# Optimization experiments

Hardware: AMD Instinct MI355X
Metric: run time of the kernel (lower is better)

Reference implementation:

```python
import jax, jax.numpy as jnp
import numpy as np

N = 100000            # number of nodes
E = 1600000           # number of edges (avg degree 16)
D = 32                # embedding dim
MASK_DEPTH = 3        # cfg.mask_depth
PATH_PROB = 0.5       # cfg.path_prob
NUM_MASK_CAND = 1024  # cfg.num_mask_cand
EPS_NORM = 1e-12      # F.normalize eps


def setup_inputs() -> dict:
    key = jax.random.key(0)
    k1, k2 = jax.random.split(key)
    edge_index = jax.random.randint(k1, (2, E), 0, N)  # [2, E] (row, col) COO indices
    adj_values = jnp.ones((E,), dtype=jnp.float32)     # sparse values (binary adjacency)
    embeds = jax.random.normal(k2, (N, D), dtype=jnp.float32)
    return {"edge_index": edge_index, "adj_values": adj_values, "embeds": embeds}


def _spmm(rows, cols, vals, x):
    # out[i] = sum_{e: rows[e]==i} vals[e] * x[cols[e]]  -- irregular gather + scatter-add
    return jax.ops.segment_sum(x[cols] * vals[:, None], rows, num_segments=N)


def _l2_normalize(x):
    n = jnp.sqrt(jnp.sum(x * x, axis=-1, keepdims=True))
    return x / jnp.maximum(n, EPS_NORM)


def reference(edge_index, adj_values, embeds):
    rows, cols = edge_index[0], edge_index[1]
    vals = adj_values

    # order = row-sums of sparse adj, shape [N, 1]
    order = jax.ops.segment_sum(vals, rows, num_segments=N)[:, None]

    fst_emb = _spmm(rows, cols, vals, embeds) - embeds
    fst_num = order
    emb = [fst_emb]
    num = [fst_num]

    drop_key = jax.random.key(42)
    for i in range(MASK_DEPTH):
        # sparse_dropout with keep prob path_prob**(i+1); zeroing values == dropping edges in spmm
        keep_prob = PATH_PROB ** (i + 1)
        u = jax.random.uniform(jax.random.fold_in(drop_key, i), (E,))
        keep = jnp.floor(u + keep_prob)  # 1.0 with prob keep_prob, else 0.0
        vals = vals * keep               # dropout compounds across iterations

        emb.append(_spmm(rows, cols, vals, emb[-1]) - emb[-1] - order * emb[-1])
        num.append(_spmm(rows, cols, vals, num[-1]) - num[-1] - order)
        order = jax.ops.segment_sum(vals, rows, num_segments=N)[:, None]

    subgraph_embeds = sum(emb) / (sum(num) + 1e-8)
    subgraph_embeds = _l2_normalize(subgraph_embeds)
    embeds_n = _l2_normalize(embeds)

    scores = jnp.sum(subgraph_embeds * embeds_n, axis=-1)  # [N]
    # Gumbel noise: -log(-log(U))
    u = jax.random.uniform(jax.random.key(7), (N,))
    scores = scores + (-jnp.log(-jnp.log(u)))

    _, candidates = jax.lax.top_k(scores, NUM_MASK_CAND)
    return scores, candidates
```

## Files before the change

kernel.cpp:

```cpp
#include <hip/hip_runtime.h>
#include <stdint.h>
#include <stddef.h>

#define NN 100000
#define NE 1600000
#define DD 32
#define NCAND 1024
#define HSIZE 65536
#define SORTN 4096
#define NBUK ((NN + 255) / 256)
#define EPB 4096
#define BCAP 5120

#define CAP1 832000
#define CAP2 432000
#define CAP3 240000

__host__ __device__ inline void tf2x32(uint32_t k0, uint32_t k1, uint32_t x0, uint32_t x1,
                                       uint32_t& o0, uint32_t& o1) {
  uint32_t ks2 = k0 ^ k1 ^ 0x1BD11BDAu;
  uint32_t v0 = x0 + k0, v1 = x1 + k1;
#define TFR(r) { v0 += v1; v1 = (v1 << (r)) | (v1 >> (32 - (r))); v1 ^= v0; }
  TFR(13) TFR(15) TFR(26) TFR(6)   v0 += k1;  v1 += ks2 + 1u;
  TFR(17) TFR(29) TFR(16) TFR(24)  v0 += ks2; v1 += k0 + 2u;
  TFR(13) TFR(15) TFR(26) TFR(6)   v0 += k0;  v1 += k1 + 3u;
  TFR(17) TFR(29) TFR(16) TFR(24)  v0 += k1;  v1 += ks2 + 4u;
  TFR(13) TFR(15) TFR(26) TFR(6)   v0 += ks2; v1 += k0 + 5u;
#undef TFR
  o0 = v0; o1 = v1;
}

__device__ __forceinline__ uint32_t jax_bits32(uint32_t k0, uint32_t k1, uint32_t i) {
  uint32_t o0, o1;
  tf2x32(k0, k1, 0u, i, o0, o1);
  return o0 ^ o1;
}

__device__ __forceinline__ float bits_to_uniform(uint32_t b) {
  return __fsub_rn(__uint_as_float((b >> 9) | 0x3f800000u), 1.0f);
}

__device__ __forceinline__ float pairwise32(const float* x) {
  float r[8];
#pragma unroll
  for (int j = 0; j < 8; ++j) r[j] = x[j];
#pragma unroll
  for (int b = 8; b < 32; b += 8)
#pragma unroll
    for (int j = 0; j < 8; ++j) r[j] = __fadd_rn(r[j], x[b + j]);
  float a01 = __fadd_rn(r[0], r[1]), a23 = __fadd_rn(r[2], r[3]);
  float a45 = __fadd_rn(r[4], r[5]), a67 = __fadd_rn(r[6], r[7]);
  return __fadd_rn(__fadd_rn(a01, a23), __fadd_rn(a45, a67));
}


__global__ __launch_bounds__(512) void kA2_bin(
    const int* __restrict__ rows, const int* __restrict__ cols,
    const float* __restrict__ adj,
    uint32_t k00, uint32_t k01, uint32_t k10, uint32_t k11,
    uint32_t k20, uint32_t k21,
    int* __restrict__ bucketCursor, int4* __restrict__ pkBin,
    int* __restrict__ bucketCntS) {
  __shared__ int hist[NBUK];
  __shared__ int base[NBUK];
  __shared__ int h1[NBUK];
  __shared__ int h2[NBUK];
  __shared__ int h3[NBUK];
  __shared__ uint8_t lvs[EPB];
  __shared__ uint16_t rank16[EPB];
  int tid = threadIdx.x;
  for (int i = tid; i < NBUK; i += 512) { hist[i] = 0; h1[i] = 0; h2[i] = 0; h3[i] = 0; }
  __syncthreads();
  int e0 = blockIdx.x * EPB;
  for (int k = 0; k < 8; ++k) {
    int e = e0 + k * 512 + tid;
    int lv = 0;
    if (e < NE) {
      float u0 = bits_to_uniform(jax_bits32(k00, k01, (uint32_t)e));
      float u1 = bits_to_uniform(jax_bits32(k10, k11, (uint32_t)e));
      float u2 = bits_to_uniform(jax_bits32(k20, k21, (uint32_t)e));
      float kp0 = floorf(__fadd_rn(u0, 0.5f));
      float kp1 = floorf(__fadd_rn(u1, 0.25f));
      float kp2 = floorf(__fadd_rn(u2, 0.125f));
      if (kp0 != 0.0f) { lv = 1; if (kp1 != 0.0f) { lv = 2; if (kp2 != 0.0f) lv = 3; } }
      int b = rows[e] >> 8;
      rank16[k * 512 + tid] = (uint16_t)atomicAdd(&hist[b], 1);
      if (lv >= 1) {
        atomicAdd(&h1[b], 1);
        if (lv >= 2) {
          atomicAdd(&h2[b], 1);
          if (lv >= 3) atomicAdd(&h3[b], 1);
        }
      }
    }
    lvs[k * 512 + tid] = (uint8_t)lv;
  }
  __syncthreads();
  for (int i = tid; i < NBUK; i += 512) {
    int h = hist[i];
    base[i] = (h > 0) ? atomicAdd(&bucketCursor[i], h) : 0;
    if (h) atomicAdd(&bucketCntS[i], h);
    if (h1[i]) atomicAdd(&bucketCntS[NBUK + i], h1[i]);
    if (h2[i]) atomicAdd(&bucketCntS[2 * NBUK + i], h2[i]);
    if (h3[i]) atomicAdd(&bucketCntS[3 * NBUK + i], h3[i]);
  }
  __syncthreads();
  for (int k = 0; k < 8; ++k) {
    int e = e0 + k * 512 + tid;
    if (e < NE) {
      int r = rows[e];
      int b = r >> 8;
      int lv = (int)lvs[k * 512 + tid];
      int pos = base[b] + (int)rank16[k * 512 + tid];
      if (pos < BCAP)
        pkBin[(size_t)b * BCAP + pos] =
            make_int4(cols[e], __float_as_int(adj[e]), (e << 2) | lv, r);
    }
  }
}

__global__ __launch_bounds__(512) void k_scanBS(const int* __restrict__ bucketCntS,
                                                int* __restrict__ bucketBaseS) {
  __shared__ int sb[512];
  int a = blockIdx.x;
  const int* c = bucketCntS + (size_t)a * NBUK;
  int* o = bucketBaseS + (size_t)a * (NBUK + 1);
  int tid = threadIdx.x;
  int v = (tid < NBUK) ? c[tid] : 0;
  sb[tid] = v;
  __syncthreads();
  for (int off = 1; off < 512; off <<= 1) {
    int x = (tid >= off) ? sb[tid - off] : 0;
    __syncthreads();
    sb[tid] += x;
    __syncthreads();
  }
  if (tid < NBUK) o[tid] = sb[tid] - v;
  if (tid == NBUK - 1) o[NBUK] = sb[tid];
}

__global__ __launch_bounds__(512) void kB_emit(
    const int* __restrict__ bucketBaseS, const int4* __restrict__ pkBin,
    int* __restrict__ rpAll,
    int2* __restrict__ pk0, int2* __restrict__ pk1,
    int2* __restrict__ pk2, int2* __restrict__ pk3,
    float* __restrict__ order0, float* __restrict__ order1, float* __restrict__ order2) {
  __shared__ unsigned long long cnt64[256];
  __shared__ unsigned long long sb64[256];
  __shared__ unsigned long long ps64[512];
  __shared__ int start0[256];
  __shared__ int cur[256];
  __shared__ uint32_t keyF[BCAP];
  __shared__ int2 payL[BCAP];
  __shared__ uint16_t origG[BCAP];
  int b = blockIdx.x, tid = threadIdx.x;
  int bB0 = bucketBaseS[b];
  int n = bucketBaseS[b + 1] - bB0;
  if (n > BCAP) n = BCAP;
  size_t sRead = (size_t)b * BCAP;
  int r0 = b << 8;
  int nr = NN - r0; if (nr > 256) nr = 256;
  int bB1 = bucketBaseS[(NBUK + 1) + b];
  int bB2 = bucketBaseS[2 * (NBUK + 1) + b];
  int bB3 = bucketBaseS[3 * (NBUK + 1) + b];
  if (tid < 256) { cnt64[tid] = 0ull; cur[tid] = 0; }
  __syncthreads();
  for (int i = tid; i < n; i += 512) {
    int4 p = pkBin[sRead + i];
    int lr = p.w - r0;
    int lv = p.z & 3;
    keyF[i] = ((uint32_t)lr << 23) | (uint32_t)p.z;
    payL[i] = make_int2(p.x, p.y);
    unsigned long long add = 1ull;
    if (lv >= 1) add |= 1ull << 16;
    if (lv >= 2) add |= 1ull << 32;
    if (lv >= 3) add |= 1ull << 48;
    atomicAdd(&cnt64[lr], add);
  }
  __syncthreads();
  unsigned long long own = (tid < 256) ? cnt64[tid] : 0ull;
  if (tid < 256) sb64[tid] = own;
  __syncthreads();
  for (int off = 1; off < 256; off <<= 1) {
    unsigned long long v = (tid < 256 && tid >= off) ? sb64[tid - off] : 0ull;
    __syncthreads();
    if (tid < 256) sb64[tid] += v;
    __syncthreads();
  }
  if (tid < 256) {
    unsigned long long ex = sb64[tid] - own;
    start0[tid] = (int)(ex & 0xFFFFull);
    if (tid < nr) {
      rpAll[r0 + tid] = bB0 + (int)(ex & 0xFFFFull);
      rpAll[(NN + 1) + r0 + tid] = bB1 + (int)((ex >> 16) & 0xFFFFull);
      rpAll[2 * (NN + 1) + r0 + tid] = bB2 + (int)((ex >> 32) & 0xFFFFull);
      rpAll[3 * (NN + 1) + r0 + tid] = bB3 + (int)((ex >> 48) & 0xFFFFull);
    }
  }
  if (b == NBUK - 1 && tid == 0) {
    rpAll[NN] = bucketBaseS[NBUK];
    rpAll[(NN + 1) + NN] = bucketBaseS[(NBUK + 1) + NBUK];
    rpAll[2 * (NN + 1) + NN] = bucketBaseS[2 * (NBUK + 1) + NBUK];
    rpAll[3 * (NN + 1) + NN] = bucketBaseS[3 * (NBUK + 1) + NBUK];
  }
  __syncthreads();
  for (int i = tid; i < n; i += 512) {
    int lr = (int)(keyF[i] >> 23);
    int slot = start0[lr] + atomicAdd(&cur[lr], 1);
    origG[slot] = (uint16_t)i;
  }
  __syncthreads();
  {
    int C2 = (n + 511) >> 9;
    int lo2 = tid * C2, hi2 = lo2 + C2;
    if (lo2 > n) lo2 = n;
    if (hi2 > n) hi2 = n;
    uint16_t vals[10];
    uint16_t pos[10];
    int cntE = 0;
    for (int i = lo2; i < hi2; ++i) {
      uint16_t ov = origG[i];
      uint32_t ki = keyF[ov];
      int lr = (int)(ki >> 23);
      int st = start0[lr];
      int d = (int)(cnt64[lr] & 0xFFFFull);
      int rank = 0;
      for (int j = 0; j < d; ++j) {
        uint32_t kj = keyF[origG[st + j]];
        rank += (kj < ki) ? 1 : 0;
      }
      vals[cntE] = ov;
      pos[cntE] = (uint16_t)(st + rank);
      ++cntE;
    }
    __syncthreads();
    for (int q = 0; q < cntE; ++q) origG[pos[q]] = vals[q];
  }
  __syncthreads();
  if (tid < nr) {
    int d = (int)(cnt64[tid] & 0xFFFFull);
    int st = start0[tid];
    float o0 = 0.0f, o1v = 0.0f, o2v = 0.0f;
    for (int i = 0; i < d; ++i) {
      uint16_t o = origG[st + i];
      int lv = (int)(keyF[o] & 3u);
      float a = __int_as_float(payL[o].y);
      o0 = __fadd_rn(o0, a);
      if (lv >= 1) { o1v = __fadd_rn(o1v, a); if (lv >= 2) o2v = __fadd_rn(o2v, a); }
    }
    order0[r0 + tid] = o0; order1[r0 + tid] = o1v; order2[r0 + tid] = o2v;
  }
  int C = (n + 511) >> 9;
  int lo = tid * C, hi = lo + C;
  if (lo > n) lo = n;
  if (hi > n) hi = n;
  int c1 = 0, c2 = 0, c3 = 0;
  for (int i = lo; i < hi; ++i) {
    int lv = (int)(keyF[origG[i]] & 3u);
    c1 += (lv >= 1); c2 += (lv >= 2); c3 += (lv >= 3);
  }
  unsigned long long mine = (unsigned long long)c1 |
                            ((unsigned long long)c2 << 16) |
                            ((unsigned long long)c3 << 32);
  ps64[tid] = mine;
  __syncthreads();
  for (int off = 1; off < 512; off <<= 1) {
    unsigned long long v = (tid >= off) ? ps64[tid - off] : 0ull;
    __syncthreads();
    ps64[tid] += v;
    __syncthreads();
  }
  unsigned long long ex = ps64[tid] - mine;
  int o1 = bB1 + (int)(ex & 0xFFFFull);
  int o2 = bB2 + (int)((ex >> 16) & 0xFFFFull);
  int o3 = bB3 + (int)((ex >> 32) & 0xFFFFull);
  for (int i = lo; i < hi; ++i) {
    uint16_t o = origG[i];
    int lv = (int)(keyF[o] & 3u);
    int2 pkv = payL[o];
    pk0[bB0 + i] = pkv;
    if (lv >= 1) {
      pk1[o1++] = pkv;
      if (lv >= 2) {
        pk2[o2++] = pkv;
        if (lv >= 3) pk3[o3++] = pkv;
      }
    }
  }
}


__global__ void k_emb0(const int* __restrict__ rp, const int2* __restrict__ pk,
                       const float* __restrict__ embeds, float* __restrict__ e0) {
  int tid = blockIdx.x * blockDim.x + threadIdx.x;
  int r = tid >> 5, d = tid & 31;
  if (r >= NN) return;
  int s = rp[r], t = rp[r + 1];
  float acc = 0.0f;
  for (int base = s; base < t; base += 32) {
    int idx = base + d;
    int2 p = (idx < t) ? pk[idx] : make_int2(0, 0);
    int m = t - base; if (m > 32) m = 32;
    for (int j = 0; j < m; j += 8) {
      int cc[8], aa[8];
      float xx[8];
#pragma unroll
      for (int q = 0; q < 8; ++q) {
        cc[q] = __shfl(p.x, j + q, 32);
        aa[q] = __shfl(p.y, j + q, 32);
      }
#pragma unroll
      for (int q = 0; q < 8; ++q) xx[q] = embeds[(size_t)cc[q] * DD + d];
#pragma unroll
      for (int q = 0; q < 8; ++q)
        acc = __fadd_rn(acc, __fmul_rn(__int_as_float(aa[q]), xx[q]));
    }
  }
  e0[(size_t)r * DD + d] = __fsub_rn(acc, embeds[(size_t)r * DD + d]);
}

__global__ void k_emb_step(const int* __restrict__ rp, const int2* __restrict__ pk,
                           const float* __restrict__ ord, const float* __restrict__ ecur,
                           float* __restrict__ enext, float* __restrict__ esum,
                           const float* __restrict__ ncur, float* __restrict__ nnext,
                           float* __restrict__ nsum, int mode) {
  int tid = blockIdx.x * blockDim.x + threadIdx.x;
  int r = tid >> 5, d = tid & 31;
  if (r >= NN) return;
  int s = rp[r], t = rp[r + 1];
  float acc = 0.0f, accn = 0.0f;
  for (int base = s; base < t; base += 32) {
    int idx = base + d;
    int2 p = (idx < t) ? pk[idx] : make_int2(0, 0);
    int m = t - base; if (m > 32) m = 32;
    for (int j = 0; j < m; j += 8) {
      int cc[8], aa[8];
      float xx[8], nn[8];
#pragma unroll
      for (int q = 0; q < 8; ++q) {
        cc[q] = __shfl(p.x, j + q, 32);
        aa[q] = __shfl(p.y, j + q, 32);
      }
#pragma unroll
      for (int q = 0; q < 8; ++q) {
        xx[q] = ecur[(size_t)cc[q] * DD + d];
        nn[q] = ncur[cc[q]];
      }
#pragma unroll
      for (int q = 0; q < 8; ++q) {
        float av = __int_as_float(aa[q]);
        acc = __fadd_rn(acc, __fmul_rn(av, xx[q]));
        accn = __fadd_rn(accn, __fmul_rn(av, nn[q]));
      }
    }
  }
  float ordv = ord[r];
  size_t idx = (size_t)r * DD + d;
  float ec = ecur[idx];
  float o = __fsub_rn(__fsub_rn(acc, ec), __fmul_rn(ordv, ec));
  if (mode != 3) enext[idx] = o;
  if (mode == 1) esum[idx] = __fadd_rn(ec, o);
  else esum[idx] = __fadd_rn(esum[idx], o);
  if (d == 0) {
    float nc = ncur[r];
    float on = __fsub_rn(__fsub_rn(accn, nc), ordv);
    if (mode != 3) nnext[r] = on;
    if (mode == 1) nsum[r] = __fadd_rn(nc, on);
    else nsum[r] = __fadd_rn(nsum[r], on);
  }
}

__global__ void k_final(const float* __restrict__ embeds, const float* __restrict__ emb_sum,
                        const float* __restrict__ num_sum, uint32_t gk0, uint32_t gk1,
                        float* __restrict__ out_scores, int* __restrict__ hist) {
  int r = blockIdx.x * blockDim.x + threadIdx.x;
  if (r >= NN) return;
  float denom = __fadd_rn(num_sum[r], 1e-8f);
  float sub[DD], em[DD], pr[DD];
  const float4* ps = (const float4*)(emb_sum + (size_t)r * DD);
  const float4* pe = (const float4*)(embeds + (size_t)r * DD);
#pragma unroll
  for (int j = 0; j < 8; ++j) {
    float4 a = ps[j], b = pe[j];
    sub[4 * j + 0] = __fdiv_rn(a.x, denom); sub[4 * j + 1] = __fdiv_rn(a.y, denom);
    sub[4 * j + 2] = __fdiv_rn(a.z, denom); sub[4 * j + 3] = __fdiv_rn(a.w, denom);
    em[4 * j + 0] = b.x; em[4 * j + 1] = b.y; em[4 * j + 2] = b.z; em[4 * j + 3] = b.w;
  }
#pragma unroll
  for (int d = 0; d < DD; ++d) pr[d] = __fmul_rn(sub[d], sub[d]);
  float n1 = fmaxf(__fsqrt_rn(pairwise32(pr)), 1e-12f);
#pragma unroll
  for (int d = 0; d < DD; ++d) pr[d] = __fmul_rn(em[d], em[d]);
  float n2 = fmaxf(__fsqrt_rn(pairwise32(pr)), 1e-12f);
#pragma unroll
  for (int d = 0; d < DD; ++d)
    pr[d] = __fmul_rn(__fdiv_rn(sub[d], n1), __fdiv_rn(em[d], n2));
  float dot = pairwise32(pr);
  float u = bits_to_uniform(jax_bits32(gk0, gk1, (uint32_t)r));
  float l1 = (float)log((double)u);
  float w = -l1;
  float l2 = (float)log((double)w);
  float g = -l2;
  float score = __fadd_rn(dot, g);
  out_scores[r] = score;
  uint32_t kb = __float_as_uint(score);
  kb = (kb & 0x80000000u) ? ~kb : (kb | 0x80000000u);
  atomicAdd(&hist[kb >> 16], 1);
}

__global__ void k_cutoff(const int* __restrict__ hist, int* __restrict__ cutoff) {
  __shared__ int psum[1024];
  int t = threadIdx.x;
  int base = HSIZE - (t + 1) * 64;
  int own = 0;
  for (int i = 0; i < 64; ++i) own += hist[base + i];
  psum[t] = own;
  __syncthreads();
  for (int off = 1; off < 1024; off <<= 1) {
    int v = (t >= off) ? psum[t - off] : 0;
    __syncthreads();
    psum[t] += v;
    __syncthreads();
  }
  int incl = psum[t];
  int prev = incl - own;
  if (incl >= NCAND && prev < NCAND) {
    int c = prev;
    int b = HSIZE - t * 64 - 1;
    while (b >= base) {
      c += hist[b];
      if (c >= NCAND) break;
      --b;
    }
    *cutoff = b;
  }
}

__global__ void k_collect(const float* __restrict__ scores, const int* __restrict__ cutoff,
                          unsigned long long* __restrict__ buf, int* __restrict__ cnt2) {
  int r = blockIdx.x * blockDim.x + threadIdx.x;
  if (r >= NN) return;
  uint32_t kb = __float_as_uint(scores[r]);
  kb = (kb & 0x80000000u) ? ~kb : (kb | 0x80000000u);
  if ((int)(kb >> 16) >= *cutoff) {
    int p = atomicAdd(cnt2, 1);
    if (p < SORTN)
      buf[p] = ((unsigned long long)kb << 32) | (uint32_t)(~(uint32_t)r);
  }
}

__global__ __launch_bounds__(1024) void k_sort(const unsigned long long* __restrict__ buf,
                                               const int* __restrict__ cnt2,
                                               float* __restrict__ out_cand) {
  __shared__ unsigned long long s[SORTN];
  int m = *cnt2;
  if (m > SORTN) m = SORTN;
  for (int i = threadIdx.x; i < SORTN; i += 1024) s[i] = (i < m) ? buf[i] : 0ull;
  __syncthreads();
  for (int k = 2; k <= SORTN; k <<= 1) {
    for (int j = k >> 1; j > 0; j >>= 1) {
      for (int i = threadIdx.x; i < SORTN; i += 1024) {
        int ixj = i ^ j;
        if (ixj > i) {
          unsigned long long a = s[i], b = s[ixj];
          bool desc = ((i & k) == 0);
          if (desc ? (a < b) : (a > b)) { s[i] = b; s[ixj] = a; }
        }
      }
      __syncthreads();
    }
  }
  for (int i = threadIdx.x; i < NCAND; i += 1024) {
    uint32_t idx = ~((uint32_t)(s[i] & 0xffffffffull));
    out_cand[i] = (float)idx;
  }
}

extern "C" void kernel_launch(void* const* d_in, const int* in_sizes, int n_in,
                              void* d_out, int out_size, void* d_ws, size_t ws_size,
                              hipStream_t stream) {
  const int* rows = (const int*)d_in[0];
  const int* cols = rows + NE;
  const float* adj = (const float*)d_in[1];
  const float* embeds = (const float*)d_in[2];
  float* out = (float*)d_out;

  char* p = (char*)d_ws;
  auto alloc = [&](size_t bytes) {
    char* q = p;
    p += (bytes + 255) & ~(size_t)255;
    return q;
  };
  size_t zero_bytes = (size_t)(5 * NBUK + HSIZE + 8) * 4;
  char* zero_base = (char*)alloc(zero_bytes);
  int* bucketCursor = (int*)zero_base;
  int* bucketCntS = bucketCursor + NBUK;
  int* hist = bucketCntS + 4 * NBUK;
  int* cnt2 = hist + HSIZE;

  int* bucketBaseS = (int*)alloc((size_t)4 * (NBUK + 1) * 4);
  int* rpAll = (int*)alloc((size_t)4 * (NN + 1) * 4);
  size_t padBytes = (size_t)NBUK * BCAP * 16;
  char* unionAB = (char*)alloc(padBytes);
  int4* pkBin = (int4*)unionAB;
  float* embA = (float*)unionAB;
  float* embB = (float*)(unionAB + (size_t)NN * DD * 4);
  int2* pk0 = (int2*)alloc((size_t)NE * 8);
  int2* pk1 = (int2*)alloc((size_t)CAP1 * 8);
  int2* pk2 = (int2*)alloc((size_t)CAP2 * 8);
  int2* pk3 = (int2*)alloc((size_t)CAP3 * 8);
  float* embS = (float*)alloc((size_t)NN * DD * 4);
  float* order0 = (float*)alloc(NN * 4);
  float* order1 = (float*)alloc(NN * 4);
  float* order2 = (float*)alloc(NN * 4);
  float* num1 = (float*)alloc(NN * 4);
  float* num2 = (float*)alloc(NN * 4);
  float* numS = (float*)alloc(NN * 4);
  unsigned long long* buf = (unsigned long long*)alloc(SORTN * 8);

  uint32_t dk[3][2];
  for (int i = 0; i < 3; ++i) tf2x32(0u, 42u, 0u, (uint32_t)i, dk[i][0], dk[i][1]);

  hipMemsetAsync(zero_base, 0, zero_bytes, stream);

  int gE = (NE + EPB - 1) / EPB;
  kA2_bin<<<gE, 512, 0, stream>>>(rows, cols, adj, dk[0][0], dk[0][1], dk[1][0], dk[1][1],
                                  dk[2][0], dk[2][1], bucketCursor, pkBin, bucketCntS);
  k_scanBS<<<4, 512, 0, stream>>>(bucketCntS, bucketBaseS);
  kB_emit<<<NBUK, 512, 0, stream>>>(bucketBaseS, pkBin, rpAll,
                                    pk0, pk1, pk2, pk3, order0, order1, order2);

  const int* rp0 = rpAll;
  const int* rp1 = rpAll + (NN + 1);
  const int* rp2 = rpAll + 2 * (NN + 1);
  const int* rp3 = rpAll + 3 * (NN + 1);

  int gEmb = (NN * 32 + 255) / 256;
  k_emb0<<<gEmb, 256, 0, stream>>>(rp0, pk0, embeds, embA);

  k_emb_step<<<gEmb, 256, 0, stream>>>(rp1, pk1, order0, embA, embB, embS,
                                       order0, num1, numS, 1);
  k_emb_step<<<gEmb, 256, 0, stream>>>(rp2, pk2, order1, embB, embA, embS,
                                       num1, num2, numS, 2);
  k_emb_step<<<gEmb, 256, 0, stream>>>(rp3, pk3, order2, embA, embB, embS,
                                       num2, num1, numS, 3);

  k_final<<<(NN + 255) / 256, 256, 0, stream>>>(embeds, embS, numS, 0u, 7u, out, hist);
  k_cutoff<<<1, 1024, 0, stream>>>(hist, cnt2 + 1);
  k_collect<<<(NN + 255) / 256, 256, 0, stream>>>(out, cnt2 + 1, buf, cnt2);
  k_sort<<<1, 1024, 0, stream>>>(buf, cnt2, out + NN);
}
```

Before: 375.3 us.

## Replace single-block bitonic sort with multi-block rank-by-counting top-k selection

```diff
diff --git a/kernel.cpp b/kernel.cpp
--- a/kernel.cpp
+++ b/kernel.cpp
@@ -449,30 +449,28 @@
   }
 }
 
-__global__ __launch_bounds__(1024) void k_sort(const unsigned long long* __restrict__ buf,
-                                               const int* __restrict__ cnt2,
-                                               float* __restrict__ out_cand) {
+__global__ __launch_bounds__(256) void k_rank(const unsigned long long* __restrict__ buf,
+                                              const int* __restrict__ cnt2,
+                                              float* __restrict__ out_cand) {
   __shared__ unsigned long long s[SORTN];
   int m = *cnt2;
   if (m > SORTN) m = SORTN;
-  for (int i = threadIdx.x; i < SORTN; i += 1024) s[i] = (i < m) ? buf[i] : 0ull;
-  __syncthreads();
-  for (int k = 2; k <= SORTN; k <<= 1) {
-    for (int j = k >> 1; j > 0; j >>= 1) {
-      for (int i = threadIdx.x; i < SORTN; i += 1024) {
-        int ixj = i ^ j;
-        if (ixj > i) {
-          unsigned long long a = s[i], b = s[ixj];
-          bool desc = ((i & k) == 0);
-          if (desc ? (a < b) : (a > b)) { s[i] = b; s[ixj] = a; }
-        }
-      }
-      __syncthreads();
-    }
-  }
-  for (int i = threadIdx.x; i < NCAND; i += 1024) {
-    uint32_t idx = ~((uint32_t)(s[i] & 0xffffffffull));
-    out_cand[i] = (float)idx;
+  if (blockIdx.x * 256 >= m) return;
+  for (int i = threadIdx.x; i < m; i += 256) s[i] = buf[i];
+  __syncthreads();
+  int i = blockIdx.x * 256 + threadIdx.x;
+  if (i >= m) return;
+  unsigned long long mine = s[i];
+  int rank = 0;
+  int j = 0;
+  for (; j + 8 <= m; j += 8) {
+#pragma unroll
+    for (int q = 0; q < 8; ++q) rank += (s[j + q] > mine) ? 1 : 0;
+  }
+  for (; j < m; ++j) rank += (s[j] > mine) ? 1 : 0;
+  if (rank < NCAND) {
+    uint32_t idx = ~((uint32_t)(mine & 0xffffffffull));
+    out_cand[rank] = (float)idx;
   }
 }
 
@@ -548,5 +546,5 @@
   k_final<<<(NN + 255) / 256, 256, 0, stream>>>(embeds, embS, numS, 0u, 7u, out, hist);
   k_cutoff<<<1, 1024, 0, stream>>>(hist, cnt2 + 1);
   k_collect<<<(NN + 255) / 256, 256, 0, stream>>>(out, cnt2 + 1, buf, cnt2);
-  k_sort<<<1, 1024, 0, stream>>>(buf, cnt2, out + NN);
-}
+  k_rank<<<(SORTN + 255) / 256, 256, 0, stream>>>(buf, cnt2, out + NN);
+}
```

After: 343.8 us. 8.4% less time.
